# Optimization experiments

Measured on AMD Instinct MI355X. Metric: run time of the kernel, lower is better.

The kernel has to match this reference:

```python
import jax, jax.numpy as jnp
import numpy as np

NEG_SLOPE = 0.2  # LeakyReLU slope

N, E, D_IN, D_OUT, H, NBIN = 50000, 500000, 256, 256, 8, 10
DH = D_OUT // H


def setup_inputs() -> dict:
    key = jax.random.key(0)
    ks = jax.random.split(key, 9)
    emb_rel = jax.random.normal(ks[0], (N, D_IN), dtype=jnp.float32)
    head_idxs = jax.random.randint(ks[1], (E,), 0, N, dtype=jnp.int32)
    tail_idxs = jax.random.randint(ks[2], (E,), 0, N, dtype=jnp.int32)
    bins = jax.random.randint(ks[3], (E,), 0, NBIN, dtype=jnp.int32)
    # xavier-normal-ish scaled params (gain for relu)
    attn_proj_w = jax.random.normal(ks[4], (D_OUT, 2 * D_IN), dtype=jnp.float32) * (1.4142 * (2.0 / (2 * D_IN + D_OUT)) ** 0.5)
    attn_proj_b = jnp.zeros((D_OUT,), dtype=jnp.float32)
    attn_bin = jax.random.normal(ks[5], (NBIN, H, 1), dtype=jnp.float32) * 0.3
    attn_vec = jax.random.normal(ks[6], (1, H, DH), dtype=jnp.float32) * (1.4142 * (2.0 / (H + DH)) ** 0.5)
    aggr_proj_w = jax.random.normal(ks[7], (D_OUT, D_IN), dtype=jnp.float32) * (1.4142 * (2.0 / (D_IN + D_OUT)) ** 0.5)
    aggr_proj_b = jnp.zeros((D_OUT,), dtype=jnp.float32)
    return {
        "emb_rel": emb_rel,
        "head_idxs": head_idxs,
        "tail_idxs": tail_idxs,
        "bins": bins,
        "attn_proj_w": attn_proj_w,
        "attn_proj_b": attn_proj_b,
        "attn_bin": attn_bin,
        "attn_vec": attn_vec,
        "aggr_proj_w": aggr_proj_w,
        "aggr_proj_b": aggr_proj_b,
        "num_nodes": N,
    }


def reference(emb_rel, head_idxs, tail_idxs, bins, attn_proj_w, attn_proj_b,
              attn_bin, attn_vec, aggr_proj_w, aggr_proj_b, num_nodes):
    num_head, dim_hid = attn_vec.shape[1], attn_vec.shape[2]
    eh = emb_rel[head_idxs]                      # (E, D_in)
    et = emb_rel[tail_idxs]                      # (E, D_in)
    concat = jnp.concatenate([eh, et], axis=-1)  # (E, 2*D_in)
    proj = (concat @ attn_proj_w.T + attn_proj_b).reshape(-1, num_head, dim_hid)
    lrelu = jnp.where(proj >= 0, proj, NEG_SLOPE * proj)
    # raw attention logits per edge/head: (E, H, 1)
    attn_raw = jnp.sum(lrelu * attn_vec, axis=-1, keepdims=True) + attn_bin[bins]
    # segmented softmax over edges grouped by head node
    seg_max = jax.ops.segment_max(attn_raw, head_idxs, num_segments=num_nodes)
    seg_max = jnp.where(jnp.isfinite(seg_max), seg_max, 0.0)  # empty segments -> 0 (never gathered anyway)
    attn_val = jnp.exp(attn_raw - seg_max[head_idxs])
    attn_sums = jax.ops.segment_sum(attn_val, head_idxs, num_segments=num_nodes)
    beta = attn_val / (attn_sums[head_idxs] + 1e-16)            # (E, H, 1)
    aggr = (et @ aggr_proj_w.T + aggr_proj_b).reshape(-1, num_head, dim_hid)
    out = jax.ops.segment_sum(beta * aggr, head_idxs, num_segments=num_nodes)
    return out.reshape(num_nodes, num_head * dim_hid)
```

## Files before the change

kernel.cpp:

```cpp
#include <hip/hip_runtime.h>
#include <math.h>

#define D_IN 256
#define D_OUT 256
#define NH 8
#define DH 32
#define NBIN 10
#define NEG_SLOPE 0.2f
#define CAP 96
#define LOG2E 1.4426950408889634f
#define THR 8.0f

typedef short short4v __attribute__((ext_vector_type(4)));
typedef short short8 __attribute__((ext_vector_type(8)));
typedef float f32x4 __attribute__((ext_vector_type(4)));

__device__ __forceinline__ unsigned short f2bf(float f) {
  unsigned u = __float_as_uint(f);
  unsigned r = u + 0x7fffu + ((u >> 16) & 1u);
  return (unsigned short)(r >> 16);
}
__device__ __forceinline__ float bf2f(unsigned short s) {
  return __uint_as_float((unsigned)s << 16);
}

__device__ __forceinline__ void gload16(const void* g, void* l) {
  __builtin_amdgcn_global_load_lds(
      (const __attribute__((address_space(1))) unsigned int*)g,
      (__attribute__((address_space(3))) unsigned int*)l, 16, 0, 0);
}

__global__ void prep_kernel(const float* __restrict__ attn_w,
                            const float* __restrict__ attn_b,
                            const float* __restrict__ aggr_w,
                            const float* __restrict__ aggr_b,
                            const float* __restrict__ emb,
                            unsigned short* __restrict__ WCbf,
                            float* __restrict__ biasC,
                            unsigned short* __restrict__ embbf,
                            int* __restrict__ cnt, int N) {
  const int b = blockIdx.x, k = threadIdx.x;
  if (b < 768) {
    const int j = b;
    int idx0 = j * 256 + k;
    if (idx0 < N) cnt[idx0] = 0;
    float v, bia = 0.f;
    if (j < 256) {
      v = attn_w[j * 512 + k];
    } else {
      int idx = j - 256, g = idx >> 3, r = idx & 7;
      if (r < 4) { int c = g * 4 + r;     v = attn_w[c * 512 + 256 + k]; bia = attn_b[c]; }
      else       { int c = g * 4 + r - 4; v = aggr_w[c * 256 + k];       bia = aggr_b[c]; }
    }
    WCbf[j * 256 + k] = f2bf(v);
    if (k == 0) biasC[j] = bia;
  } else {
    const long long total = (long long)N * 256;
    long long i = (((long long)(b - 768)) * 256 + k) * 8;
    if (i >= total) return;
    float4 a = *(const float4*)(emb + i);
    float4 c = *(const float4*)(emb + i + 4);
    short8 o;
    o[0] = (short)f2bf(a.x); o[1] = (short)f2bf(a.y);
    o[2] = (short)f2bf(a.z); o[3] = (short)f2bf(a.w);
    o[4] = (short)f2bf(c.x); o[5] = (short)f2bf(c.y);
    o[6] = (short)f2bf(c.z); o[7] = (short)f2bf(c.w);
    *(short8*)(embbf + i) = o;
  }
}

#define EPAD 36
__global__ __launch_bounds__(256) void gemm_scatter_kernel(
    const unsigned short* __restrict__ Abf,
    const unsigned short* __restrict__ Bbf,
    const float* __restrict__ biasC,
    unsigned short* __restrict__ P1bf, unsigned short* __restrict__ P2A,
    const int* __restrict__ head, const int* __restrict__ tail,
    const int* __restrict__ bins, int* __restrict__ cnt,
    int* __restrict__ bucket, int N, int E, int nscb, int nrt) {
  const int tid = threadIdx.x;
  const int b = blockIdx.x;
  if (b < nscb) {
    int e = b * 256 + tid;
    if (e < E) {
      int h = head[e];
      int slot = atomicAdd(&cnt[h], 1);
      if (slot < CAP) bucket[(size_t)h * CAP + slot] = (bins[e] << 16) | tail[e];
    }
    return;
  }
  __shared__ char smem[49152];
  float* Ls = (float*)smem;
  const int gb = b - nscb;
  const int row0 = (gb % nrt) * 128, col0 = (gb / nrt) * 256;
  const int wave = tid >> 6, l = tid & 63;
  const int wm = wave >> 1, wn = wave & 1;
  const int lr = l & 15;
  const int lq = l >> 4;
  const int srow = tid >> 2;
  const int sk = (tid & 3) * 8;
  int ar0 = row0 + srow;      if (ar0 >= N) ar0 = N - 1;
  int ar1 = row0 + 64 + srow; if (ar1 >= N) ar1 = N - 1;
  const unsigned short* pa0 = Abf + (size_t)ar0 * 256 + sk;
  const unsigned short* pa1 = Abf + (size_t)ar1 * 256 + sk;
  const unsigned short* pb0 = Bbf + (size_t)(col0 + srow) * 256 + sk;
  const unsigned short* pb1 = Bbf + (size_t)(col0 + 64 + srow) * 256 + sk;
  const unsigned short* pb2 = Bbf + (size_t)(col0 + 128 + srow) * 256 + sk;
  const unsigned short* pb3 = Bbf + (size_t)(col0 + 192 + srow) * 256 + sk;

  auto STAGE = [&](int buf, int kk) {
    unsigned short* base = (unsigned short*)(smem + buf * 24576);
    gload16(pa0 + kk, base + wave * 512);
    gload16(pa1 + kk, base + 2048 + wave * 512);
    gload16(pb0 + kk, base + 4096 + wave * 512);
    gload16(pb1 + kk, base + 6144 + wave * 512);
    gload16(pb2 + kk, base + 8192 + wave * 512);
    gload16(pb3 + kk, base + 10240 + wave * 512);
  };

  f32x4 acc[4][8] = {};
  STAGE(0, 0);
  __syncthreads();
  int cur = 0;
  for (int t = 0; t < 8; ++t) {
    if (t < 7) STAGE(cur ^ 1, (t + 1) * 32);
    __builtin_amdgcn_sched_barrier(0);
    const unsigned short* As = (const unsigned short*)(smem + cur * 24576);
    const unsigned short* Bs = As + 4096;
    short8 af[4], bfr[8];
#pragma unroll
    for (int i = 0; i < 4; ++i)
      af[i] = *(const short8*)&As[(wm * 64 + i * 16 + lr) * 32 + lq * 8];
#pragma unroll
    for (int j = 0; j < 8; ++j)
      bfr[j] = *(const short8*)&Bs[(wn * 128 + j * 16 + lr) * 32 + lq * 8];
#pragma unroll
    for (int i = 0; i < 4; ++i)
#pragma unroll
      for (int j = 0; j < 8; ++j)
        acc[i][j] = __builtin_amdgcn_mfma_f32_16x16x32_bf16(af[i], bfr[j], acc[i][j], 0, 0, 0);
    __syncthreads();
    cur ^= 1;
  }
  for (int j = 0; j < 8; ++j) {
    __syncthreads();
    const float bias = biasC[col0 + wn * 128 + j * 16 + lr];
#pragma unroll
    for (int i = 0; i < 4; ++i) {
      const int lrow = wm * 64 + i * 16 + lq * 4;
#pragma unroll
      for (int r = 0; r < 4; ++r)
        Ls[(lrow + r) * EPAD + wn * 16 + lr] = acc[i][j][r] + bias;
    }
    __syncthreads();
    const int o = tid & 3, half = o >> 1, part = o & 1;
#pragma unroll
    for (int s = 0; s < 2; ++s) {
      const int row = (tid >> 2) + s * 64;
      const int grow = row0 + row;
      if (grow < N) {
        const float* src = &Ls[row * EPAD + half * 16 + part * 8];
        short8 v;
#pragma unroll
        for (int q = 0; q < 8; ++q) v[q] = (short)f2bf(src[q]);
        const int colb = half * 128 + j * 16 + part * 8;
        if (col0 == 0)
          *(short8*)(P1bf + (size_t)grow * 256 + colb) = v;
        else
          *(short8*)(P2A + (size_t)grow * 512 + (col0 - 256) + colb) = v;
      }
    }
  }
}

template <int PAT>
__device__ __forceinline__ float swz_add(float s) {
  return s + __uint_as_float(
      (unsigned)__builtin_amdgcn_ds_swizzle((int)__float_as_uint(s), PAT));
}

__device__ __forceinline__ short8 ldP2A(const unsigned short* __restrict__ P2A,
                                        int t, int l8) {
  return *(const short8*)(P2A + ((size_t)(t & 0xFFFF) << 9) + l8);
}

__device__ __forceinline__ float edge_dot(short8 c, float4 p1, float4 av) {
  float x, s;
  x = p1.x + bf2f((unsigned short)c[0]); s  = fmaxf(x, NEG_SLOPE * x) * av.x;
  x = p1.y + bf2f((unsigned short)c[1]); s += fmaxf(x, NEG_SLOPE * x) * av.y;
  x = p1.z + bf2f((unsigned short)c[2]); s += fmaxf(x, NEG_SLOPE * x) * av.z;
  x = p1.w + bf2f((unsigned short)c[3]); s += fmaxf(x, NEG_SLOPE * x) * av.w;
  s = swz_add<0x041F>(s);
  s = swz_add<0x081F>(s);
  s = swz_add<0x101F>(s);
  return s;
}

__device__ __forceinline__ float4 edge_val(short8 c) {
  float4 v;
  v.x = bf2f((unsigned short)c[4]); v.y = bf2f((unsigned short)c[5]);
  v.z = bf2f((unsigned short)c[6]); v.w = bf2f((unsigned short)c[7]);
  return v;
}

__global__ __launch_bounds__(128) void node_aggr_kernel(
    const unsigned short* __restrict__ P1bf, const unsigned short* __restrict__ P2A,
    const int* __restrict__ cnt, const int* __restrict__ bucket,
    const float* __restrict__ attn_vec, const float* __restrict__ attn_bin,
    float* __restrict__ out, int N) {
  __shared__ float sbin[NBIN * NH];
  const int tid = threadIdx.x;
  if (tid < NBIN * NH) sbin[tid] = attn_bin[tid] * LOG2E;
  __syncthreads();
  const int nu = __builtin_amdgcn_readfirstlane(blockIdx.x * 2 + (tid >> 6));
  if (nu >= N) return;
  const int l = tid & 63;
  const int l8 = l * 8;
  const int h = l >> 3;
  float4 av = *(const float4*)(attn_vec + l * 4);
  av.x *= LOG2E; av.y *= LOG2E; av.z *= LOG2E; av.w *= LOG2E;
  const short4v p1s = *(const short4v*)(P1bf + (size_t)nu * 256 + l * 4);
  float4 p1;
  p1.x = bf2f((unsigned short)p1s[0]); p1.y = bf2f((unsigned short)p1s[1]);
  p1.z = bf2f((unsigned short)p1s[2]); p1.w = bf2f((unsigned short)p1s[3]);
  const int* brow = bucket + (size_t)nu * CAP;
  int d = cnt[nu];
  if (d > CAP) d = CAP;
  float m = 0.f, m8 = 0.f, sum = 0.f;
  float4 acc = make_float4(0.f, 0.f, 0.f, 0.f);
  if (d > 0) {
    const int dm1 = d - 1;
    const int t0 = brow[0];
    short8 c0 = ldP2A(P2A, t0, l8);
    int ta[4];
    short8 ca[4];
#pragma unroll
    for (int k = 0; k < 4; ++k) {
      const int ja = (1 + k <= dm1) ? 1 + k : dm1;
      ta[k] = brow[ja];
      ca[k] = ldP2A(P2A, ta[k], l8);
    }
    __builtin_amdgcn_sched_barrier(0);
    m = edge_dot(c0, p1, av) + sbin[(t0 >> 16) * NH + h];
    m8 = m + THR;
    sum = 1.f;
    const float4 v0 = edge_val(c0);
    acc.x = v0.x; acc.y = v0.y; acc.z = v0.z; acc.w = v0.w;
    int i = 1;
#pragma unroll 2
    for (; i + 3 < d; i += 4) {
      int tn[4];
      short8 cn[4];
#pragma unroll
      for (int k = 0; k < 4; ++k) {
        const int jn = (i + 4 + k <= dm1) ? i + 4 + k : dm1;
        tn[k] = brow[jn];
        cn[k] = ldP2A(P2A, tn[k], l8);
      }
      __builtin_amdgcn_sched_barrier(0);
      float lg[4];
#pragma unroll
      for (int k = 0; k < 4; ++k)
        lg[k] = edge_dot(ca[k], p1, av) + sbin[(ta[k] >> 16) * NH + h];
      const float lmax = fmaxf(fmaxf(lg[0], lg[1]), fmaxf(lg[2], lg[3]));
      if (__any(lmax > m8)) {
        const float mn = fmaxf(m, lmax);
        const float sc = __builtin_amdgcn_exp2f(m - mn);
        sum *= sc; acc.x *= sc; acc.y *= sc; acc.z *= sc; acc.w *= sc;
        m = mn; m8 = mn + THR;
      }
#pragma unroll
      for (int k = 0; k < 4; ++k) {
        const float w = __builtin_amdgcn_exp2f(lg[k] - m);
        const float4 v = edge_val(ca[k]);
        sum += w;
        acc.x += w * v.x; acc.y += w * v.y;
        acc.z += w * v.z; acc.w += w * v.w;
      }
#pragma unroll
      for (int k = 0; k < 4; ++k) { ta[k] = tn[k]; ca[k] = cn[k]; }
    }
    const int r = d - i;
#pragma unroll
    for (int k = 0; k < 3; ++k) {
      if (k < r) {
        const float lgk = edge_dot(ca[k], p1, av) + sbin[(ta[k] >> 16) * NH + h];
        if (__any(lgk > m8)) {
          const float mn = fmaxf(m, lgk);
          const float sc = __builtin_amdgcn_exp2f(m - mn);
          sum *= sc; acc.x *= sc; acc.y *= sc; acc.z *= sc; acc.w *= sc;
          m = mn; m8 = mn + THR;
        }
        const float w = __builtin_amdgcn_exp2f(lgk - m);
        const float4 v = edge_val(ca[k]);
        sum += w;
        acc.x += w * v.x; acc.y += w * v.y;
        acc.z += w * v.z; acc.w += w * v.w;
      }
    }
  }
  const float inv = 1.f / (sum + 1e-16f);
  float4 o;
  o.x = acc.x * inv; o.y = acc.y * inv; o.z = acc.z * inv; o.w = acc.w * inv;
  *(float4*)(out + (size_t)nu * 256 + l * 4) = o;
}

extern "C" void kernel_launch(void* const* d_in, const int* in_sizes, int n_in,
                              void* d_out, int out_size, void* d_ws, size_t ws_size,
                              hipStream_t stream) {
  const float* emb      = (const float*)d_in[0];
  const int*   head     = (const int*)d_in[1];
  const int*   tail     = (const int*)d_in[2];
  const int*   bins     = (const int*)d_in[3];
  const float* attn_w   = (const float*)d_in[4];
  const float* attn_b   = (const float*)d_in[5];
  const float* attn_bin = (const float*)d_in[6];
  const float* attn_vec = (const float*)d_in[7];
  const float* aggr_w   = (const float*)d_in[8];
  const float* aggr_b   = (const float*)d_in[9];
  float* out = (float*)d_out;

  const int N = in_sizes[0] / D_IN;
  const int E = in_sizes[1];

  char* ws = (char*)d_ws;
  size_t off = 0;
  auto walloc = [&](size_t bytes) -> void* {
    void* p = ws + off;
    off += (bytes + 255) & ~(size_t)255;
    return p;
  };
  unsigned short* P1bf   = (unsigned short*)walloc((size_t)N * 256 * sizeof(short));
  unsigned short* P2A    = (unsigned short*)walloc((size_t)N * 512 * sizeof(short));
  unsigned short* embbf  = (unsigned short*)walloc((size_t)N * 256 * sizeof(short));
  unsigned short* WCbf   = (unsigned short*)walloc((size_t)768 * 256 * sizeof(short));
  float*          biasC  = (float*)walloc(768 * sizeof(float));
  int*            cnt    = (int*)walloc((size_t)N * sizeof(int));
  int*            bucket = (int*)walloc((size_t)N * CAP * sizeof(int));

  const int conv_blocks = (int)(((long long)N * 256 / 8 + 255) / 256);
  prep_kernel<<<768 + conv_blocks, 256, 0, stream>>>(attn_w, attn_b, aggr_w, aggr_b,
                                                     emb, WCbf, biasC, embbf, cnt, N);

  const int nscb = (E + 255) / 256;
  const int nrt = (N + 127) / 128;
  gemm_scatter_kernel<<<nscb + nrt * 3, 256, 0, stream>>>(
      embbf, WCbf, biasC, P1bf, P2A, head, tail, bins, cnt, bucket,
      N, E, nscb, nrt);

  node_aggr_kernel<<<(N + 1) / 2, 128, 0, stream>>>(P1bf, P2A, cnt, bucket,
                                                    attn_vec, attn_bin, out, N);
}
```

Measured before the change: 267.1 us.

## Deepen GEMM prefetch pipeline with manual waitcnt and put scatter blocks last

The GEMM main loop now issues two stages up front and refills a buffer only after its fragments are read into registers. Manual vmcnt/lgkmcnt waits and raw s_barrier calls replace __syncthreads, so global loads overlap the MFMA work instead of being serialized by full barriers. Bias values are hoisted into registers before the loop, and the bucket-scatter blocks are moved after the GEMM blocks in the grid so the heavy tiles get scheduled first. The hand-tuned vmcnt counts depend on the exact number of loads per STAGE and are fragile if that changes.

Measured after the change: 274.5 us. 1.03x slower.

```diff
diff --git a/kernel.cpp b/kernel.cpp
--- a/kernel.cpp
+++ b/kernel.cpp
@@ -77,11 +77,11 @@
     unsigned short* __restrict__ P1bf, unsigned short* __restrict__ P2A,
     const int* __restrict__ head, const int* __restrict__ tail,
     const int* __restrict__ bins, int* __restrict__ cnt,
-    int* __restrict__ bucket, int N, int E, int nscb, int nrt) {
+    int* __restrict__ bucket, int N, int E, int ngemm, int nrt) {
   const int tid = threadIdx.x;
   const int b = blockIdx.x;
-  if (b < nscb) {
-    int e = b * 256 + tid;
+  if (b >= ngemm) {
+    int e = (b - ngemm) * 256 + tid;
     if (e < E) {
       int h = head[e];
       int slot = atomicAdd(&cnt[h], 1);
@@ -91,8 +91,7 @@
   }
   __shared__ char smem[49152];
   float* Ls = (float*)smem;
-  const int gb = b - nscb;
-  const int row0 = (gb % nrt) * 128, col0 = (gb / nrt) * 256;
+  const int row0 = (b % nrt) * 128, col0 = (b / nrt) * 256;
   const int wave = tid >> 6, l = tid & 63;
   const int wm = wave >> 1, wn = wave & 1;
   const int lr = l & 15;
@@ -108,6 +107,11 @@
   const unsigned short* pb2 = Bbf + (size_t)(col0 + 128 + srow) * 256 + sk;
   const unsigned short* pb3 = Bbf + (size_t)(col0 + 192 + srow) * 256 + sk;
 
+  float biasr[8];
+#pragma unroll
+  for (int j = 0; j < 8; ++j) biasr[j] = biasC[col0 + wn * 128 + j * 16 + lr];
+  asm volatile("s_waitcnt vmcnt(0)" ::: "memory");
+
   auto STAGE = [&](int buf, int kk) {
     unsigned short* base = (unsigned short*)(smem + buf * 24576);
     gload16(pa0 + kk, base + wave * 512);
@@ -120,12 +124,14 @@
 
   f32x4 acc[4][8] = {};
   STAGE(0, 0);
-  __syncthreads();
-  int cur = 0;
+  STAGE(1, 32);
+#pragma unroll
   for (int t = 0; t < 8; ++t) {
-    if (t < 7) STAGE(cur ^ 1, (t + 1) * 32);
+    if (t < 7) { asm volatile("s_waitcnt vmcnt(6)" ::: "memory"); }
+    else       { asm volatile("s_waitcnt vmcnt(0)" ::: "memory"); }
     __builtin_amdgcn_sched_barrier(0);
-    const unsigned short* As = (const unsigned short*)(smem + cur * 24576);
+    __builtin_amdgcn_s_barrier();
+    const unsigned short* As = (const unsigned short*)(smem + (t & 1) * 24576);
     const unsigned short* Bs = As + 4096;
     short8 af[4], bfr[8];
 #pragma unroll
@@ -134,23 +140,25 @@
 #pragma unroll
     for (int j = 0; j < 8; ++j)
       bfr[j] = *(const short8*)&Bs[(wn * 128 + j * 16 + lr) * 32 + lq * 8];
+    asm volatile("s_waitcnt lgkmcnt(0)" ::: "memory");
+    __builtin_amdgcn_sched_barrier(0);
+    __builtin_amdgcn_s_barrier();
+    if (t < 6) STAGE(t & 1, (t + 2) * 32);
+    __builtin_amdgcn_sched_barrier(0);
 #pragma unroll
     for (int i = 0; i < 4; ++i)
 #pragma unroll
       for (int j = 0; j < 8; ++j)
         acc[i][j] = __builtin_amdgcn_mfma_f32_16x16x32_bf16(af[i], bfr[j], acc[i][j], 0, 0, 0);
-    __syncthreads();
-    cur ^= 1;
   }
   for (int j = 0; j < 8; ++j) {
     __syncthreads();
-    const float bias = biasC[col0 + wn * 128 + j * 16 + lr];
 #pragma unroll
     for (int i = 0; i < 4; ++i) {
       const int lrow = wm * 64 + i * 16 + lq * 4;
 #pragma unroll
       for (int r = 0; r < 4; ++r)
-        Ls[(lrow + r) * EPAD + wn * 16 + lr] = acc[i][j][r] + bias;
+        Ls[(lrow + r) * EPAD + wn * 16 + lr] = acc[i][j][r] + biasr[j];
     }
     __syncthreads();
     const int o = tid & 3, half = o >> 1, part = o & 1;
@@ -342,11 +350,12 @@
   prep_kernel<<<768 + conv_blocks, 256, 0, stream>>>(attn_w, attn_b, aggr_w, aggr_b,
                                                      emb, WCbf, biasC, embbf, cnt, N);
 
+  const int nrt = (N + 127) / 128;
+  const int ngemm = nrt * 3;
   const int nscb = (E + 255) / 256;
-  const int nrt = (N + 127) / 128;
-  gemm_scatter_kernel<<<nscb + nrt * 3, 256, 0, stream>>>(
+  gemm_scatter_kernel<<<ngemm + nscb, 256, 0, stream>>>(
       embbf, WCbf, biasC, P1bf, P2A, head, tail, bins, cnt, bucket,
-      N, E, nscb, nrt);
+      N, E, ngemm, nrt);
 
   node_aggr_kernel<<<(N + 1) / 2, 128, 0, stream>>>(P1bf, P2A, cnt, bucket,
                                                     attn_vec, attn_bin, out, N);
```
